# Optimization experiments

Measured on AMD Instinct MI355X. Metric: run time of the kernel, lower is better.

The kernel has to match this reference:

```python
import jax, jax.numpy as jnp
import numpy as np

NUM_LAYERS = 4
INPUT_SIZE = 80
D_MODEL = 512
NHEAD = 8
D_FF = 2048
B = 16
S_MAX = 512
LN_EPS = 1e-5


def setup_inputs() -> dict:
    key = jax.random.key(0)
    ks = jax.random.split(key, 16)
    L, D, F, I = NUM_LAYERS, D_MODEL, D_FF, INPUT_SIZE
    s = 0.02
    inp = {
        "x": jax.random.normal(ks[0], (B, S_MAX, I), dtype=jnp.float32),
        "lens": jax.random.randint(ks[1], (B,), S_MAX // 2, S_MAX + 1, dtype=jnp.int32),
        "We": jax.random.normal(ks[2], (D, I), jnp.float32) * s,
        "be": jnp.zeros((D,), jnp.float32),
        "Wqkv": jax.random.normal(ks[3], (L, 3 * D, D), jnp.float32) * s,
        "bqkv": jnp.zeros((L, 3 * D), jnp.float32),
        "Wo": jax.random.normal(ks[4], (L, D, D), jnp.float32) * s,
        "bo": jnp.zeros((L, D), jnp.float32),
        "ln1_g": jnp.ones((L, D), jnp.float32),
        "ln1_b": jnp.zeros((L, D), jnp.float32),
        "W1": jax.random.normal(ks[5], (L, F, D), jnp.float32) * s,
        "b1": jnp.zeros((L, F), jnp.float32),
        "W2": jax.random.normal(ks[6], (L, D, F), jnp.float32) * s,
        "b2": jnp.zeros((L, D), jnp.float32),
        "ln2_g": jnp.ones((L, D), jnp.float32),
        "ln2_b": jnp.zeros((L, D), jnp.float32),
    }
    return inp


def _layer_norm(x, g, b):
    m = jnp.mean(x, axis=-1, keepdims=True)
    v = jnp.mean(jnp.square(x - m), axis=-1, keepdims=True)
    return (x - m) * jax.lax.rsqrt(v + LN_EPS) * g + b


def _pos_encoding(S, D, dtype):
    pos = jnp.arange(S, dtype=jnp.float32)[:, None]
    div = jnp.exp(jnp.arange(0, D, 2, dtype=jnp.float32) * (-np.log(10000.0) / D))
    pe = jnp.zeros((S, D), jnp.float32)
    pe = pe.at[:, 0::2].set(jnp.sin(pos * div))
    pe = pe.at[:, 1::2].set(jnp.cos(pos * div))
    return pe.astype(dtype)


def _encoder_layer(h, key_mask, Wqkv, bqkv, Wo, bo, g1, b1_, W1, b1f, W2, b2f, g2, b2_):
    # h: [B,S,D], key_mask: [B,S] bool (True = valid). Post-norm (PyTorch default).
    Bq, S, D = h.shape
    dh = D // NHEAD
    qkv = jnp.einsum("bsd,ed->bse", h, Wqkv) + bqkv  # [B,S,3D]
    q, k, v = jnp.split(qkv, 3, axis=-1)
    q = q.reshape(Bq, S, NHEAD, dh).transpose(0, 2, 1, 3)
    k = k.reshape(Bq, S, NHEAD, dh).transpose(0, 2, 1, 3)
    v = v.reshape(Bq, S, NHEAD, dh).transpose(0, 2, 1, 3)
    scores = jnp.einsum("bhqd,bhkd->bhqk", q, k) / jnp.sqrt(jnp.asarray(dh, h.dtype))
    scores = jnp.where(key_mask[:, None, None, :], scores, jnp.asarray(-1e9, h.dtype))
    attn = jax.nn.softmax(scores, axis=-1)
    ctx = jnp.einsum("bhqk,bhkd->bhqd", attn, v)
    ctx = ctx.transpose(0, 2, 1, 3).reshape(Bq, S, D)
    attn_out = jnp.einsum("bsd,ed->bse", ctx, Wo) + bo
    h = _layer_norm(h + attn_out, g1, b1_)
    ff = jnp.einsum("bsf,df->bsd", jax.nn.relu(jnp.einsum("bsd,fd->bsf", h, W1) + b1f), W2) + b2f
    return _layer_norm(h + ff, g2, b2_)


def reference(x, lens, We, be, Wqkv, bqkv, Wo, bo, ln1_g, ln1_b, W1, b1, W2, b2, ln2_g, ln2_b):
    Bq, S, _ = x.shape
    D = We.shape[0]
    h = jnp.einsum("bsi,di->bsd", x, We) + be  # Linear embedding
    h = h + _pos_encoding(S, D, h.dtype)[None]
    key_mask = jnp.arange(S)[None, :] < lens[:, None]  # [B,S]
    for l in range(Wqkv.shape[0]):
        h = _encoder_layer(h, key_mask, Wqkv[l], bqkv[l], Wo[l], bo[l],
                           ln1_g[l], ln1_b[l], W1[l], b1[l], W2[l], b2[l],
                           ln2_g[l], ln2_b[l])
    pooled = jnp.sum(h * key_mask[..., None].astype(h.dtype), axis=1)
    pooled = pooled / lens[:, None].astype(h.dtype)  # mean over valid tokens
    return pooled, lens
```

## Files before the change

kernel.cpp:

```cpp
#include <hip/hip_runtime.h>
#include <math.h>

#define D_MODEL 512
#define NHEAD   8
#define DH      64
#define D_FF    2048
#define BATCH   16
#define SMAX    512
#define NTOK    (BATCH*SMAX)
#define NLAYER  4

constexpr int MODE_RELU = 3;
constexpr int MODE_PART = 4;

typedef __attribute__((ext_vector_type(8))) __bf16 bf16x8;
typedef __attribute__((ext_vector_type(4))) float  f32x4;
typedef __attribute__((ext_vector_type(8))) int    i32x8;
typedef unsigned char u8;

#define WSCALE_INV 0.03125f
#define QSCALE     0.18033688011112042f

__device__ __forceinline__ unsigned short f2bf(float f) {
  union { float f; unsigned u; } v; v.f = f;
  unsigned r = v.u + 0x7FFFu + ((v.u >> 16) & 1u);
  return (unsigned short)(r >> 16);
}
__device__ __forceinline__ float bf2f(unsigned short u) {
  union { unsigned u; float f; } v; v.u = ((unsigned)u) << 16; return v.f;
}
__device__ __forceinline__ int pk4(float a, float b, float c, float d) {
  int t = __builtin_amdgcn_cvt_pk_fp8_f32(a, b, 0, false);
  t = __builtin_amdgcn_cvt_pk_fp8_f32(c, d, t, true);
  return t;
}

__device__ __forceinline__ void gl_lds16(const unsigned short* g, unsigned short* l) {
  __builtin_amdgcn_global_load_lds(
      (const __attribute__((address_space(1))) unsigned int*)g,
      (__attribute__((address_space(3)))       unsigned int*)l, 16, 0, 0);
}
__device__ __forceinline__ void gl_lds16b(const u8* g, u8* l) {
  __builtin_amdgcn_global_load_lds(
      (const __attribute__((address_space(1))) unsigned int*)g,
      (__attribute__((address_space(3)))       unsigned int*)l, 16, 0, 0);
}

__device__ __forceinline__ i32x8 ldfrag(const u8* base, int row, int q) {
  const int rx = row & 7;
  const int4 lo = *(const int4*)(base + (row << 7) + ((((2*q)    ) ^ rx) << 4));
  const int4 hi = *(const int4*)(base + (row << 7) + ((((2*q) + 1) ^ rx) << 4));
  union { int4 p[2]; i32x8 v; } u;
  u.p[0] = lo; u.p[1] = hi;
  return u.v;
}

template<int MODE>
__global__ __launch_bounds__(256)
void gemm_fp8(const u8* __restrict__ A, const u8* __restrict__ Bw,
              const float* __restrict__ bias, u8* __restrict__ C8,
              unsigned short* __restrict__ Cb,
              const int* __restrict__ lens, int K, int CK, int N)
{
  const int lin = blockIdx.x + gridDim.x*(blockIdx.y + gridDim.y*blockIdx.z);
  int m0, n0, kz = 0;
  {
    m0 = (lin % gridDim.y) * 128;
    const int rest = lin / gridDim.y;
    n0 = (rest % gridDim.x) * 128;
    kz = rest / gridDim.x;
  }
  if ((m0 & 511) >= lens[m0 >> 9]) return;

  __shared__ __attribute__((aligned(16))) u8 As[2][16384];
  __shared__ __attribute__((aligned(16))) u8 Bs[2][16384];
  const int tid  = threadIdx.x;
  const int lane = tid & 63;
  const int w    = tid >> 6;
  const int wm   = (w & 1) * 64;
  const int wn   = (w >> 1) * 64;
  const int l15  = lane & 15, quad = lane >> 4;

  f32x4 acc[4][4] = {};

  const int sr  = tid >> 3;
  const int sch = ((tid & 7) ^ (sr & 7)) * 16;
  const u8* Ag = A  + (long)(m0 + sr) * K + kz*CK + sch;
  const u8* Bg = Bw + (long)(n0 + sr) * K + kz*CK + sch;
  const long rowskip = (long)32 * K;
  const int t16 = tid * 16;
  const int niter = CK >> 7;

  auto stage = [&](int t, int bix) {
    const u8* a_ = Ag + t*128;
    const u8* b_ = Bg + t*128;
#pragma unroll
    for (int s = 0; s < 4; s++) {
      gl_lds16b(a_ + s*rowskip, &As[bix][s*4096 + t16]);
      gl_lds16b(b_ + s*rowskip, &Bs[bix][s*4096 + t16]);
    }
  };

  stage(0, 0);
  stage(1, 1);

  for (int it = 0; it < niter; ++it) {
    if (it + 1 < niter)
      asm volatile("s_waitcnt vmcnt(8)\n\ts_barrier" ::: "memory");
    else
      asm volatile("s_waitcnt vmcnt(0)\n\ts_barrier" ::: "memory");

    const int cur = it & 1;
    const u8* Ac = &As[cur][0];
    const u8* Bc = &Bs[cur][0];

    i32x8 bfv[4];
#pragma unroll
    for (int j = 0; j < 4; j++)
      bfv[j] = ldfrag(Bc, wn + j*16 + l15, quad);
#pragma unroll
    for (int i = 0; i < 4; i++) {
      const i32x8 af = ldfrag(Ac, wm + i*16 + l15, quad);
#pragma unroll
      for (int j = 0; j < 4; j++)
        acc[i][j] = __builtin_amdgcn_mfma_scale_f32_16x16x128_f8f6f4(
            af, bfv[j], acc[i][j], 0, 0, 0, 0x7F7F7F7F, 0, 0x7F7F7F7F);
    }

    if (it + 2 < niter) {
      __syncthreads();
      stage(it + 2, cur);
    }
  }

  __syncthreads();
  const int rr8 = lane >> 3, ch8 = lane & 7;

  if (MODE == MODE_RELU) {
    float* epf = (float*)&As[0][0] + w * 1088;
#pragma unroll
    for (int i = 0; i < 4; i++) {
#pragma unroll
      for (int j = 0; j < 4; j++) {
        const float cbv = bias[n0 + wn + j*16 + l15];
#pragma unroll
        for (int r = 0; r < 4; r++)
          epf[(quad*4 + r)*68 + j*16 + l15] = fmaxf(acc[i][j][r]*WSCALE_INV + cbv, 0.f);
      }
      asm volatile("s_waitcnt lgkmcnt(0)" ::: "memory");
      const int row = lane >> 2, c16 = (lane & 3) * 16;
      const float* rp = epf + row*68 + c16;
      f32x4 f0 = *(const f32x4*)(rp + 0);
      f32x4 f1 = *(const f32x4*)(rp + 4);
      f32x4 f2 = *(const f32x4*)(rp + 8);
      f32x4 f3 = *(const f32x4*)(rp + 12);
      int4 o;
      o.x = pk4(f0.x, f0.y, f0.z, f0.w);
      o.y = pk4(f1.x, f1.y, f1.z, f1.w);
      o.z = pk4(f2.x, f2.y, f2.z, f2.w);
      o.w = pk4(f3.x, f3.y, f3.z, f3.w);
      const int mrow = m0 + wm + i*16 + row;
      *(int4*)&C8[(long)mrow*N + n0 + wn + c16] = o;
      asm volatile("s_waitcnt lgkmcnt(0)" ::: "memory");
    }
  } else {
    unsigned short* epi = (unsigned short*)&As[0][0] + w * 1152;
#pragma unroll
    for (int i = 0; i < 4; i++) {
#pragma unroll
      for (int j = 0; j < 4; j++) {
#pragma unroll
        for (int r = 0; r < 4; r++) {
          float v = acc[i][j][r] * WSCALE_INV;
          epi[(quad*4 + r)*72 + j*16 + l15] = f2bf(v);
        }
      }
      asm volatile("s_waitcnt lgkmcnt(0)" ::: "memory");
#pragma unroll
      for (int rs = 0; rs < 2; rs++) {
        const int row  = rs*8 + rr8;
        const int mrow = m0 + wm + i*16 + row;
        bf16x8 val = *(const bf16x8*)&epi[row*72 + ch8*8];
        *(bf16x8*)&Cb[((long)kz*NTOK + mrow)*N + n0 + wn + ch8*8] = val;
      }
      asm volatile("s_waitcnt lgkmcnt(0)" ::: "memory");
    }
  }
}

__global__ __launch_bounds__(256)
void gemm_qkv(const u8* __restrict__ h8, const u8* __restrict__ wq,
              const float* __restrict__ bqkv,
              unsigned short* __restrict__ qd, unsigned short* __restrict__ kd,
              unsigned short* __restrict__ vt_b,
              const int* __restrict__ lens)
{
  const int lin = blockIdx.x;
  const bool isVT = lin >= 512;
  int m0, n0;
  if (isVT) { const int idx = lin - 512; n0 = (idx & 63) * 128; m0 = (idx >> 6) * 128; }
  else      { m0 = (lin & 63) * 128;     n0 = (lin >> 6) * 128; }
  { const int tb = isVT ? n0 : m0;
    if ((tb & 511) >= lens[tb >> 9]) return; }

  const u8* Ap = isVT ? (wq + (long)2*D_MODEL*D_MODEL) : h8;
  const u8* Bp = isVT ? h8 : wq;

  __shared__ __attribute__((aligned(16))) u8 As[2][16384];
  __shared__ __attribute__((aligned(16))) u8 Bs[2][16384];
  const int tid  = threadIdx.x;
  const int lane = tid & 63;
  const int w    = tid >> 6;
  const int wm   = (w & 1) * 64;
  const int wn   = (w >> 1) * 64;
  const int l15  = lane & 15, quad = lane >> 4;

  f32x4 acc[4][4] = {};

  const int sr  = tid >> 3;
  const int sch = ((tid & 7) ^ (sr & 7)) * 16;
  const u8* Ag = Ap + (long)(m0 + sr) * 512 + sch;
  const u8* Bg = Bp + (long)(n0 + sr) * 512 + sch;
  const long rowskip = (long)32 * 512;
  const int t16 = tid * 16;

  auto stage = [&](int t, int bix) {
    const u8* a_ = Ag + t*128;
    const u8* b_ = Bg + t*128;
#pragma unroll
    for (int s = 0; s < 4; s++) {
      gl_lds16b(a_ + s*rowskip, &As[bix][s*4096 + t16]);
      gl_lds16b(b_ + s*rowskip, &Bs[bix][s*4096 + t16]);
    }
  };

  stage(0, 0);
  stage(1, 1);

#pragma unroll 1
  for (int it = 0; it < 4; ++it) {
    if (it + 1 < 4)
      asm volatile("s_waitcnt vmcnt(8)\n\ts_barrier" ::: "memory");
    else
      asm volatile("s_waitcnt vmcnt(0)\n\ts_barrier" ::: "memory");

    const int cur = it & 1;
    const u8* Ac = &As[cur][0];
    const u8* Bc = &Bs[cur][0];

    i32x8 bfv[4];
#pragma unroll
    for (int j = 0; j < 4; j++)
      bfv[j] = ldfrag(Bc, wn + j*16 + l15, quad);
#pragma unroll
    for (int i = 0; i < 4; i++) {
      const i32x8 af = ldfrag(Ac, wm + i*16 + l15, quad);
#pragma unroll
      for (int j = 0; j < 4; j++)
        acc[i][j] = __builtin_amdgcn_mfma_scale_f32_16x16x128_f8f6f4(
            af, bfv[j], acc[i][j], 0, 0, 0, 0x7F7F7F7F, 0, 0x7F7F7F7F);
    }

    if (it + 2 < 4) {
      __syncthreads();
      stage(it + 2, cur);
    }
  }

  __syncthreads();
  const int rr8 = lane >> 3, ch8 = lane & 7;
  unsigned short* epi = (unsigned short*)&As[0][0] + w * 1152;
  const bool isq = !isVT && (((n0 + wn) >> 9) == 0);
#pragma unroll
  for (int i = 0; i < 4; i++) {
    float rbv[4];
    if (isVT) {
#pragma unroll
      for (int r = 0; r < 4; r++) rbv[r] = bqkv[2*D_MODEL + m0 + wm + i*16 + quad*4 + r];
    }
#pragma unroll
    for (int j = 0; j < 4; j++) {
      float cbv = 0.f;
      if (!isVT) cbv = bqkv[n0 + wn + j*16 + l15];
#pragma unroll
      for (int r = 0; r < 4; r++) {
        float v = acc[i][j][r] * WSCALE_INV;
        if (!isVT) { v += cbv; if (isq) v *= QSCALE; }
        else       v += rbv[r];
        epi[(quad*4 + r)*72 + j*16 + l15] = f2bf(v);
      }
    }
    asm volatile("s_waitcnt lgkmcnt(0)" ::: "memory");
#pragma unroll
    for (int rs = 0; rs < 2; rs++) {
      const int row  = rs*8 + rr8;
      const int mrow = m0 + wm + i*16 + row;
      bf16x8 val = *(const bf16x8*)&epi[row*72 + ch8*8];
      if (!isVT) {
        const int nb    = n0 + wn;
        const int which = nb >> 9;
        const int head  = (nb >> 6) & 7;
        unsigned short* dst = which ? kd : qd;
        const int bh = (mrow >> 9)*8 + head;
        *(bf16x8*)&dst[((long)(bh*512 + (mrow & 511)))*64 + ch8*8] = val;
      } else {
        const int head = mrow >> 6, d = mrow & 63;
        const int tok  = n0 + wn + ch8*8;
        const int b    = tok >> 9;
        *(bf16x8*)&vt_b[((long)((b*8 + head)*64 + d))*512 + (tok & 511)] = val;
      }
    }
    asm volatile("s_waitcnt lgkmcnt(0)" ::: "memory");
  }
}

template<int KS>
__global__ __launch_bounds__(256)
void reduce_ln(const unsigned short* __restrict__ part,
               const float* __restrict__ bias,
               const float* __restrict__ g, const float* __restrict__ bb,
               u8* __restrict__ h8, const int* __restrict__ lens)
{
  const int tid  = threadIdx.x;
  const int half = tid >> 7;
  const int t    = tid & 127;
  const int row  = blockIdx.x*2 + half;
  const bool valid = (row & 511) < lens[row >> 9];

  const int hv = ((const int*)(h8 + (long)row*512))[t];
  float4 bs = ((const float4*)bias)[t];
  float v0 = __builtin_amdgcn_cvt_f32_fp8(hv, 0) + bs.x;
  float v1 = __builtin_amdgcn_cvt_f32_fp8(hv, 1) + bs.y;
  float v2 = __builtin_amdgcn_cvt_f32_fp8(hv, 2) + bs.z;
  float v3 = __builtin_amdgcn_cvt_f32_fp8(hv, 3) + bs.w;
#pragma unroll
  for (int z = 0; z < KS; z++) {
    ushort4 p = ((const ushort4*)(part + ((long)z*NTOK + row)*512))[t];
    v0 += bf2f(p.x); v1 += bf2f(p.y); v2 += bf2f(p.z); v3 += bf2f(p.w);
  }
  float s  = v0 + v1 + v2 + v3;
  float s2 = v0*v0 + v1*v1 + v2*v2 + v3*v3;
#pragma unroll
  for (int off = 1; off < 64; off <<= 1) {
    s  += __shfl_xor(s, off);
    s2 += __shfl_xor(s2, off);
  }
  __shared__ float rb[2][2][2];
  if ((t & 63) == 0) { rb[half][t>>6][0] = s; rb[half][t>>6][1] = s2; }
  __syncthreads();
  s  = rb[half][0][0] + rb[half][1][0];
  s2 = rb[half][0][1] + rb[half][1][1];
  const float mean = s * (1.f/512.f);
  const float var  = fmaxf(s2 * (1.f/512.f) - mean*mean, 0.f);
  const float rstd = rsqrtf(var + 1e-5f);
  const float4 gv = ((const float4*)g)[t];
  const float4 bv = ((const float4*)bb)[t];
  const float o0 = (v0-mean)*rstd*gv.x + bv.x;
  const float o1 = (v1-mean)*rstd*gv.y + bv.y;
  const float o2 = (v2-mean)*rstd*gv.z + bv.z;
  const float o3 = (v3-mean)*rstd*gv.w + bv.w;
  if (valid)
    ((int*)(h8 + (long)row*512))[t] = pk4(o0, o1, o2, o3);
}

__global__ __launch_bounds__(256)
void attn_mfma(const unsigned short* __restrict__ qg,
               const unsigned short* __restrict__ kb,
               const unsigned short* __restrict__ vtb,
               const int* __restrict__ lens,
               u8* __restrict__ ctx8)
{
  const int bh = blockIdx.x, qt = blockIdx.y;
  const int b = bh >> 3, hh = bh & 7;
  const int len = lens[b];
  if (qt*64 >= len) return;

  __shared__ __attribute__((aligned(16))) u8 smem[41984];
  unsigned short* Ks0 = (unsigned short*)smem;
  unsigned short* Vts0 = (unsigned short*)(smem + 16384);
  unsigned short* Ps  = (unsigned short*)(smem + 32768);
  const int tid = threadIdx.x;
  const int w = tid >> 6, lane = tid & 63, l15 = lane & 15, quad = lane >> 4;
  const int t8 = tid * 8;

  const int srow = tid >> 2;
  const int s8   = (tid & 3) * 8;
  const unsigned short* Kbase = kb  + ((long)(bh*512 + srow))*64 + s8;
  const unsigned short* Vbase = vtb + ((long)(bh*64 + srow))*512 + s8;

  const unsigned short* qrow = qg + ((long)(bh*512 + qt*64 + w*16 + l15))*64;
  const bf16x8 qf0 = *(const bf16x8*)(qrow + quad*8);
  const bf16x8 qf1 = *(const bf16x8*)(qrow + 32 + quad*8);

  f32x4 O[4] = {};
  float lrow[4] = {0.f,0.f,0.f,0.f};
  unsigned short* Pw = &Ps[w*16*72];
  const int ntiles = (len + 63) >> 6;

  {
    gl_lds16(Kbase,      &Ks0[t8]);
    gl_lds16(Kbase + 32, &Ks0[2048 + t8]);
    gl_lds16(Vbase,      &Vts0[t8]);
    gl_lds16(Vbase + 32, &Vts0[2048 + t8]);
  }

  for (int kt = 0; kt < ntiles; kt++) {
    const int cur = kt & 1;
    unsigned short* Kc  = Ks0  + cur*4096;
    unsigned short* Vc  = Vts0 + cur*4096;
    __syncthreads();
    if (kt + 1 < ntiles) {
      const unsigned short* Kg = Kbase + (long)(kt+1)*64*64;
      const unsigned short* Vg = Vbase + (long)(kt+1)*64;
      unsigned short* Kn = Ks0  + (cur^1)*4096;
      unsigned short* Vn = Vts0 + (cur^1)*4096;
      gl_lds16(Kg,      &Kn[t8]);
      gl_lds16(Kg + 32, &Kn[2048 + t8]);
      gl_lds16(Vg,      &Vn[t8]);
      gl_lds16(Vg + 32, &Vn[2048 + t8]);
    }

    f32x4 sc[4];
#pragma unroll
    for (int ks = 0; ks < 4; ks++) {
      bf16x8 kf0 = *(const bf16x8*)&Kc[       (ks*16 + l15)*32 + quad*8];
      bf16x8 kf1 = *(const bf16x8*)&Kc[2048 + (ks*16 + l15)*32 + quad*8];
      f32x4 z = {};
      z = __builtin_amdgcn_mfma_f32_16x16x32_bf16(qf0, kf0, z, 0, 0, 0);
      sc[ks] = __builtin_amdgcn_mfma_f32_16x16x32_bf16(qf1, kf1, z, 0, 0, 0);
    }

    if (kt*64 + 64 > len) {
#pragma unroll
      for (int ks = 0; ks < 4; ks++) {
        const bool valid = (kt*64 + ks*16 + l15) < len;
#pragma unroll
        for (int r = 0; r < 4; r++)
          sc[ks][r] = valid ? sc[ks][r] : -1e30f;
      }
    }

    float pv[4][4];
#pragma unroll
    for (int ks = 0; ks < 4; ks++)
#pragma unroll
      for (int r = 0; r < 4; r++) {
        const float p = exp2f(sc[ks][r] - 16.f);
        pv[ks][r] = p;
        lrow[r] += p;
      }

#pragma unroll
    for (int ks = 0; ks < 4; ks++)
#pragma unroll
      for (int r = 0; r < 4; r++)
        Pw[(quad*4 + r)*72 + ks*16 + l15] = f2bf(pv[ks][r]);
    asm volatile("s_waitcnt lgkmcnt(0)" ::: "memory");

    const bf16x8 pa0 = *(const bf16x8*)&Pw[l15*72 + quad*8];
    const bf16x8 pa1 = *(const bf16x8*)&Pw[l15*72 + 32 + quad*8];
#pragma unroll
    for (int d = 0; d < 4; d++) {
      bf16x8 vf0 = *(const bf16x8*)&Vc[       (d*16 + l15)*32 + quad*8];
      bf16x8 vf1 = *(const bf16x8*)&Vc[2048 + (d*16 + l15)*32 + quad*8];
      O[d] = __builtin_amdgcn_mfma_f32_16x16x32_bf16(pa0, vf0, O[d], 0, 0, 0);
      O[d] = __builtin_amdgcn_mfma_f32_16x16x32_bf16(pa1, vf1, O[d], 0, 0, 0);
    }
  }

#pragma unroll
  for (int r = 0; r < 4; r++) {
    float t = lrow[r];
    t += __shfl_xor(t, 1);
    t += __shfl_xor(t, 2);
    t += __shfl_xor(t, 4);
    t += __shfl_xor(t, 8);
    lrow[r] = t;
  }

  __syncthreads();
  float* epf = (float*)smem + w * 1088;
#pragma unroll
  for (int r = 0; r < 4; r++) {
    const float inv = 1.f / lrow[r];
#pragma unroll
    for (int d = 0; d < 4; d++)
      epf[(quad*4 + r)*68 + d*16 + l15] = O[d][r] * inv;
  }
  asm volatile("s_waitcnt lgkmcnt(0)" ::: "memory");
  {
    const int row = lane >> 2, c16 = (lane & 3) * 16;
    const float* rp = epf + row*68 + c16;
    f32x4 f0 = *(const f32x4*)(rp + 0);
    f32x4 f1 = *(const f32x4*)(rp + 4);
    f32x4 f2 = *(const f32x4*)(rp + 8);
    f32x4 f3 = *(const f32x4*)(rp + 12);
    int4 o;
    o.x = pk4(f0.x, f0.y, f0.z, f0.w);
    o.y = pk4(f1.x, f1.y, f1.z, f1.w);
    o.z = pk4(f2.x, f2.y, f2.z, f2.w);
    o.w = pk4(f3.x, f3.y, f3.z, f3.w);
    const long gaddr = (long)(b*512 + qt*64 + w*16 + row)*512 + hh*64 + c16;
    *(int4*)&ctx8[gaddr] = o;
  }
}

__global__ __launch_bounds__(256)
void gemm_embed(const float* __restrict__ A, const float* __restrict__ Bm,
                const float* __restrict__ bias,
                u8* __restrict__ C8, int K, int N)
{
  __shared__ float As[8][132];
  __shared__ float Bs[8][68];
  const int tid = threadIdx.x;
  const int m0 = blockIdx.y * 128;
  const int n0 = blockIdx.x * 64;
  const int tx = tid & 15, ty = tid >> 4;
  const int a_k = tid & 7, a_m = tid >> 3;

  float acc[8][4] = {};
  const float* Ag = A  + (long)(m0 + a_m) * K + a_k;
  const float* Bg = Bm + (long)(n0 + a_m) * K + a_k;

  for (int k0 = 0; k0 < K; k0 += 8) {
#pragma unroll
    for (int i = 0; i < 4; i++)
      As[a_k][a_m + 32*i] = Ag[k0 + (long)32*i*K];
#pragma unroll
    for (int i = 0; i < 2; i++)
      Bs[a_k][a_m + 32*i] = Bg[k0 + (long)32*i*K];
    __syncthreads();
#pragma unroll
    for (int kk = 0; kk < 8; kk++) {
      float a[8], bv[4];
#pragma unroll
      for (int r = 0; r < 8; r++) a[r] = As[kk][ty*8 + r];
#pragma unroll
      for (int c = 0; c < 4; c++) bv[c] = Bs[kk][tx*4 + c];
#pragma unroll
      for (int r = 0; r < 8; r++)
#pragma unroll
        for (int c = 0; c < 4; c++)
          acc[r][c] += a[r] * bv[c];
    }
    __syncthreads();
  }

  const int n_base = n0 + tx*4;
  const float cfreq = -13.287712379549449f / 512.0f;
  const float dv0 = exp2f((float)(n_base)     * cfreq);
  const float dv1 = exp2f((float)(n_base + 2) * cfreq);
#pragma unroll
  for (int r = 0; r < 8; r++) {
    int m = m0 + ty*8 + r;
    int s = m & 511;
    float a0 = (float)s * dv0, a1 = (float)s * dv1;
    float s0v, c0v, s1v, c1v;
    __sincosf(a0, &s0v, &c0v);
    __sincosf(a1, &s1v, &c1v);
    int o = pk4(acc[r][0] + bias[n_base+0] + s0v,
                acc[r][1] + bias[n_base+1] + c0v,
                acc[r][2] + bias[n_base+2] + s1v,
                acc[r][3] + bias[n_base+3] + c1v);
    *(int*)(C8 + (long)m*N + n_base) = o;
  }
}

#define N4_QKV (NLAYER*3*D_MODEL*D_MODEL/4)
#define N4_WO  (NLAYER*D_MODEL*D_MODEL/4)
#define N4_W1  (NLAYER*D_FF*D_MODEL/4)
#define N4_W2  (NLAYER*D_MODEL*D_FF/4)
__global__ __launch_bounds__(256)
void cvt_all(const float* __restrict__ wq, const float* __restrict__ wo,
             const float* __restrict__ w1, const float* __restrict__ w2,
             u8* __restrict__ oq, u8* __restrict__ oo,
             u8* __restrict__ o1, u8* __restrict__ o2)
{
  int i = blockIdx.x*256 + threadIdx.x;
  const float* src; u8* dst; int off;
  if (i < N4_QKV)                          { src = wq; dst = oq; off = i; }
  else if (i < N4_QKV + N4_WO)             { src = wo; dst = oo; off = i - N4_QKV; }
  else if (i < N4_QKV + N4_WO + N4_W1)     { src = w1; dst = o1; off = i - N4_QKV - N4_WO; }
  else if (i < N4_QKV + N4_WO + N4_W1 + N4_W2) { src = w2; dst = o2; off = i - N4_QKV - N4_WO - N4_W1; }
  else return;
  float4 v = ((const float4*)src)[off];
  ((int*)dst)[off] = pk4(v.x*32.f, v.y*32.f, v.z*32.f, v.w*32.f);
}

__global__ __launch_bounds__(256)
void out_init(float* __restrict__ out, const int* __restrict__ lens)
{
  int i = blockIdx.x*256 + threadIdx.x;
  if (i < 8192) out[i] = 0.f;
  else if (i < 8192 + 16) out[i] = (float)lens[i - 8192];
}

__global__ __launch_bounds__(256)
void pool_kernel(const u8* __restrict__ h8,
                 const int* __restrict__ lens, float* __restrict__ out)
{
  const int b = blockIdx.y;
  const int s0 = blockIdx.x * 64;
  const int len = lens[b];
  if (s0 >= len) return;
  const int send = min(s0 + 64, len);
  const int tid = threadIdx.x;
  const int c = (tid & 127) * 4;
  const int half = tid >> 7;
  float a0 = 0.f, a1 = 0.f, a2 = 0.f, a3 = 0.f;
  for (int s = s0 + half; s < send; s += 2) {
    const int v = *(const int*)(h8 + ((long)(b*512 + s))*512 + c);
    a0 += __builtin_amdgcn_cvt_f32_fp8(v, 0);
    a1 += __builtin_amdgcn_cvt_f32_fp8(v, 1);
    a2 += __builtin_amdgcn_cvt_f32_fp8(v, 2);
    a3 += __builtin_amdgcn_cvt_f32_fp8(v, 3);
  }
  const float inv = 1.0f / (float)len;
  atomicAdd(out + b*512 + c + 0, a0 * inv);
  atomicAdd(out + b*512 + c + 1, a1 * inv);
  atomicAdd(out + b*512 + c + 2, a2 * inv);
  atomicAdd(out + b*512 + c + 3, a3 * inv);
}

extern "C" void kernel_launch(void* const* d_in, const int* in_sizes, int n_in,
                              void* d_out, int out_size, void* d_ws, size_t ws_size,
                              hipStream_t stream)
{
  const float* x    = (const float*)d_in[0];
  const int*   lens = (const int*)  d_in[1];
  const float* We   = (const float*)d_in[2];
  const float* be   = (const float*)d_in[3];
  const float* Wqkv = (const float*)d_in[4];
  const float* bqkv = (const float*)d_in[5];
  const float* Wo   = (const float*)d_in[6];
  const float* bo   = (const float*)d_in[7];
  const float* ln1g = (const float*)d_in[8];
  const float* ln1b = (const float*)d_in[9];
  const float* W1   = (const float*)d_in[10];
  const float* b1   = (const float*)d_in[11];
  const float* W2   = (const float*)d_in[12];
  const float* b2   = (const float*)d_in[13];
  const float* ln2g = (const float*)d_in[14];
  const float* ln2b = (const float*)d_in[15];
  float* out = (float*)d_out;

  const long TOK_D = (long)NTOK * D_MODEL;
  u8* base = (u8*)d_ws;
  u8* h8    = base + 4*TOK_D;
  u8* ctx8  = h8   + TOK_D;
  u8* ff8   = ctx8 + TOK_D;
  unsigned short* q_b  = (unsigned short*)(ff8 + 4*TOK_D);
  unsigned short* k_b  = q_b + TOK_D;
  unsigned short* vt_b = k_b + TOK_D;
  unsigned short* part = vt_b + TOK_D;
  u8* wq8 = (u8*)(part + 4*TOK_D);
  u8* wo8 = wq8 + (long)NLAYER*3*D_MODEL*D_MODEL;
  u8* w18 = wo8 + (long)NLAYER*D_MODEL*D_MODEL;
  u8* w28 = w18 + (long)NLAYER*D_FF*D_MODEL;

  const dim3 blk(256);

  {
    const int n4tot = N4_QKV + N4_WO + N4_W1 + N4_W2;
    cvt_all<<<dim3((n4tot+255)/256), blk, 0, stream>>>(
        Wqkv, Wo, W1, W2, wq8, wo8, w18, w28);
  }

  gemm_embed<<<dim3(D_MODEL/64, NTOK/128), blk, 0, stream>>>(
      x, We, be, h8, 80, D_MODEL);

  for (int l = 0; l < NLAYER; l++) {
    const u8* wq_l = wq8 + (long)l * 3*D_MODEL * D_MODEL;
    const u8* wo_l = wo8 + (long)l * D_MODEL * D_MODEL;
    const u8* w1_l = w18 + (long)l * D_FF * D_MODEL;
    const u8* w2_l = w28 + (long)l * D_MODEL * D_FF;
    const float* bqkv_l = bqkv + (long)l * 3*D_MODEL;
    const float* bo_l   = bo   + (long)l * D_MODEL;
    const float* b1_l   = b1   + (long)l * D_FF;
    const float* b2_l   = b2   + (long)l * D_MODEL;

    gemm_qkv<<<dim3(768), blk, 0, stream>>>(
        h8, wq_l, bqkv_l, q_b, k_b, vt_b, lens);

    attn_mfma<<<dim3(NHEAD*BATCH, SMAX/64), blk, 0, stream>>>(
        q_b, k_b, vt_b, lens, ctx8);

    gemm_fp8<MODE_PART><<<dim3(D_MODEL/128, NTOK/128, 2), blk, 0, stream>>>(
        ctx8, wo_l, nullptr, nullptr, part, lens,
        D_MODEL, D_MODEL/2, D_MODEL);
    reduce_ln<2><<<dim3(NTOK/2), blk, 0, stream>>>(
        part, bo_l, ln1g + l*D_MODEL, ln1b + l*D_MODEL, h8, lens);

    gemm_fp8<MODE_RELU><<<dim3(D_FF/128, NTOK/128), blk, 0, stream>>>(
        h8, w1_l, b1_l, ff8, nullptr, lens, D_MODEL, D_MODEL, D_FF);

    gemm_fp8<MODE_PART><<<dim3(D_MODEL/128, NTOK/128, 2), blk, 0, stream>>>(
        ff8, w2_l, nullptr, nullptr, part, lens,
        D_FF, D_FF/2, D_MODEL);
    reduce_ln<2><<<dim3(NTOK/2), blk, 0, stream>>>(
        part, b2_l, ln2g + l*D_MODEL, ln2b + l*D_MODEL, h8, lens);
  }

  out_init<<<dim3((8192 + 16 + 255) / 256), blk, 0, stream>>>(out, lens);
  pool_kernel<<<dim3(SMAX/64, BATCH), blk, 0, stream>>>(h8, lens, out);
}
```

Before: 502.5 us.

## Rework attention to 32x32 MFMA tiles with register-resident P and swizzled LDS

The attention kernel now handles 128 query rows per block using 32x32x16 bf16 MFMAs, halving the grid along the query dimension so each K/V tile loaded into LDS is reused by twice as many queries. Softmax probabilities stay in registers and are rearranged with v_permlane32_swap to form the A operand of the PV MFMA, removing the LDS write/read round trip for P. K/V chunks are XOR-swizzled when loaded to cut LDS bank conflicts. In exchange there are fewer blocks, so occupancy on short sequences may drop, and register pressure per thread rises.

```diff
diff --git a/kernel.cpp b/kernel.cpp
--- a/kernel.cpp
+++ b/kernel.cpp
@@ -13,9 +13,10 @@
 constexpr int MODE_RELU = 3;
 constexpr int MODE_PART = 4;
 
-typedef __attribute__((ext_vector_type(8))) __bf16 bf16x8;
-typedef __attribute__((ext_vector_type(4))) float  f32x4;
-typedef __attribute__((ext_vector_type(8))) int    i32x8;
+typedef __attribute__((ext_vector_type(8)))  __bf16 bf16x8;
+typedef __attribute__((ext_vector_type(4)))  float  f32x4;
+typedef __attribute__((ext_vector_type(16))) float  f32x16;
+typedef __attribute__((ext_vector_type(8)))  int    i32x8;
 typedef unsigned char u8;
 
 #define WSCALE_INV 0.03125f
@@ -365,7 +366,7 @@
 
 __global__ __launch_bounds__(256)
 void attn_mfma(const unsigned short* __restrict__ qg,
-               const unsigned short* __restrict__ kb,
+               const unsigned short* __restrict__ kbt,
                const unsigned short* __restrict__ vtb,
                const int* __restrict__ lens,
                u8* __restrict__ ctx8)
@@ -373,41 +374,43 @@
   const int bh = blockIdx.x, qt = blockIdx.y;
   const int b = bh >> 3, hh = bh & 7;
   const int len = lens[b];
-  if (qt*64 >= len) return;
-
-  __shared__ __attribute__((aligned(16))) u8 smem[41984];
-  unsigned short* Ks0 = (unsigned short*)smem;
+  if (qt*128 >= len) return;
+
+  __shared__ __attribute__((aligned(16))) u8 smem[35328];
+  unsigned short* Ks0  = (unsigned short*)smem;
   unsigned short* Vts0 = (unsigned short*)(smem + 16384);
-  unsigned short* Ps  = (unsigned short*)(smem + 32768);
+  float* lden = (float*)(smem + 34816);
+
   const int tid = threadIdx.x;
-  const int w = tid >> 6, lane = tid & 63, l15 = lane & 15, quad = lane >> 4;
+  const int w = tid >> 6, lane = tid & 63;
+  const int l31 = lane & 31, h = lane >> 5;
   const int t8 = tid * 8;
+  const int swz = l31 & 3;
 
   const int srow = tid >> 2;
-  const int s8   = (tid & 3) * 8;
-  const unsigned short* Kbase = kb  + ((long)(bh*512 + srow))*64 + s8;
-  const unsigned short* Vbase = vtb + ((long)(bh*64 + srow))*512 + s8;
-
-  const unsigned short* qrow = qg + ((long)(bh*512 + qt*64 + w*16 + l15))*64;
-  const bf16x8 qf0 = *(const bf16x8*)(qrow + quad*8);
-  const bf16x8 qf1 = *(const bf16x8*)(qrow + 32 + quad*8);
-
-  f32x4 O[4] = {};
-  float lrow[4] = {0.f,0.f,0.f,0.f};
-  unsigned short* Pw = &Ps[w*16*72];
+  const int spos = ((tid & 3) ^ (srow & 3)) * 8;
+  const unsigned short* Kbase = kbt + ((long)(bh*512 + srow))*64  + spos;
+  const unsigned short* Vbase = vtb + ((long)(bh*64  + srow))*512 + spos;
+
+  const unsigned short* qrow = qg + ((long)(bh*512 + qt*128 + w*32 + l31))*64 + h*8;
+  const bf16x8 qf0 = *(const bf16x8*)(qrow);
+  const bf16x8 qf1 = *(const bf16x8*)(qrow + 16);
+  const bf16x8 qf2 = *(const bf16x8*)(qrow + 32);
+  const bf16x8 qf3 = *(const bf16x8*)(qrow + 48);
+
+  f32x16 O0 = {}, O1 = {};
+  float lracc = 0.f;
   const int ntiles = (len + 63) >> 6;
 
-  {
-    gl_lds16(Kbase,      &Ks0[t8]);
-    gl_lds16(Kbase + 32, &Ks0[2048 + t8]);
-    gl_lds16(Vbase,      &Vts0[t8]);
-    gl_lds16(Vbase + 32, &Vts0[2048 + t8]);
-  }
+  gl_lds16(Kbase,      &Ks0[t8]);
+  gl_lds16(Kbase + 32, &Ks0[2048 + t8]);
+  gl_lds16(Vbase,      &Vts0[t8]);
+  gl_lds16(Vbase + 32, &Vts0[2048 + t8]);
 
   for (int kt = 0; kt < ntiles; kt++) {
     const int cur = kt & 1;
-    unsigned short* Kc  = Ks0  + cur*4096;
-    unsigned short* Vc  = Vts0 + cur*4096;
+    unsigned short* Kc = Ks0  + cur*4096;
+    unsigned short* Vc = Vts0 + cur*4096;
     __syncthreads();
     if (kt + 1 < ntiles) {
       const unsigned short* Kg = Kbase + (long)(kt+1)*64*64;
@@ -420,88 +423,100 @@
       gl_lds16(Vg + 32, &Vn[2048 + t8]);
     }
 
-    f32x4 sc[4];
-#pragma unroll
-    for (int ks = 0; ks < 4; ks++) {
-      bf16x8 kf0 = *(const bf16x8*)&Kc[       (ks*16 + l15)*32 + quad*8];
-      bf16x8 kf1 = *(const bf16x8*)&Kc[2048 + (ks*16 + l15)*32 + quad*8];
-      f32x4 z = {};
-      z = __builtin_amdgcn_mfma_f32_16x16x32_bf16(qf0, kf0, z, 0, 0, 0);
-      sc[ks] = __builtin_amdgcn_mfma_f32_16x16x32_bf16(qf1, kf1, z, 0, 0, 0);
-    }
-
-    if (kt*64 + 64 > len) {
-#pragma unroll
-      for (int ks = 0; ks < 4; ks++) {
-        const bool valid = (kt*64 + ks*16 + l15) < len;
-#pragma unroll
-        for (int r = 0; r < 4; r++)
-          sc[ks][r] = valid ? sc[ks][r] : -1e30f;
+    int dw[2][4][2];
+#pragma unroll
+    for (int kb2 = 0; kb2 < 2; kb2++) {
+      f32x16 sc = {};
+      const int krow = (kb2*32 + l31) * 32;
+      const bf16x8 af0 = *(const bf16x8*)&Kc[       krow + ((h      ^ swz) * 8)];
+      sc = __builtin_amdgcn_mfma_f32_32x32x16_bf16(af0, qf0, sc, 0, 0, 0);
+      const bf16x8 af1 = *(const bf16x8*)&Kc[       krow + (((2|h)  ^ swz) * 8)];
+      sc = __builtin_amdgcn_mfma_f32_32x32x16_bf16(af1, qf1, sc, 0, 0, 0);
+      const bf16x8 af2 = *(const bf16x8*)&Kc[2048 + krow + ((h      ^ swz) * 8)];
+      sc = __builtin_amdgcn_mfma_f32_32x32x16_bf16(af2, qf2, sc, 0, 0, 0);
+      const bf16x8 af3 = *(const bf16x8*)&Kc[2048 + krow + (((2|h)  ^ swz) * 8)];
+      sc = __builtin_amdgcn_mfma_f32_32x32x16_bf16(af3, qf3, sc, 0, 0, 0);
+
+      if (kt*64 + kb2*32 + 32 > len) {
+#pragma unroll
+        for (int r = 0; r < 16; r++) {
+          const int kk = kt*64 + kb2*32 + (r & 3) + 8*(r >> 2) + 4*h;
+          sc[r] = (kk < len) ? sc[r] : -1e30f;
+        }
       }
-    }
-
-    float pv[4][4];
-#pragma unroll
-    for (int ks = 0; ks < 4; ks++)
-#pragma unroll
-      for (int r = 0; r < 4; r++) {
-        const float p = exp2f(sc[ks][r] - 16.f);
-        pv[ks][r] = p;
-        lrow[r] += p;
+
+      float p[16];
+#pragma unroll
+      for (int r = 0; r < 16; r++) { p[r] = exp2f(sc[r] - 16.f); lracc += p[r]; }
+#pragma unroll
+      for (int rq = 0; rq < 4; rq++) {
+        dw[kb2][rq][0] = (int)f2bf(p[4*rq+0]) | ((int)f2bf(p[4*rq+1]) << 16);
+        dw[kb2][rq][1] = (int)f2bf(p[4*rq+2]) | ((int)f2bf(p[4*rq+3]) << 16);
       }
-
-#pragma unroll
-    for (int ks = 0; ks < 4; ks++)
-#pragma unroll
-      for (int r = 0; r < 4; r++)
-        Pw[(quad*4 + r)*72 + ks*16 + l15] = f2bf(pv[ks][r]);
-    asm volatile("s_waitcnt lgkmcnt(0)" ::: "memory");
-
-    const bf16x8 pa0 = *(const bf16x8*)&Pw[l15*72 + quad*8];
-    const bf16x8 pa1 = *(const bf16x8*)&Pw[l15*72 + 32 + quad*8];
-#pragma unroll
-    for (int d = 0; d < 4; d++) {
-      bf16x8 vf0 = *(const bf16x8*)&Vc[       (d*16 + l15)*32 + quad*8];
-      bf16x8 vf1 = *(const bf16x8*)&Vc[2048 + (d*16 + l15)*32 + quad*8];
-      O[d] = __builtin_amdgcn_mfma_f32_16x16x32_bf16(pa0, vf0, O[d], 0, 0, 0);
-      O[d] = __builtin_amdgcn_mfma_f32_16x16x32_bf16(pa1, vf1, O[d], 0, 0, 0);
-    }
-  }
-
-#pragma unroll
-  for (int r = 0; r < 4; r++) {
-    float t = lrow[r];
-    t += __shfl_xor(t, 1);
-    t += __shfl_xor(t, 2);
-    t += __shfl_xor(t, 4);
-    t += __shfl_xor(t, 8);
-    lrow[r] = t;
+    }
+
+#pragma unroll
+    for (int kc = 0; kc < 4; kc++) {
+      const int kb2 = kc >> 1;
+      const int rqa = (kc & 1) * 2, rqb = rqa + 1;
+      int a0 = dw[kb2][rqa][0], b0 = dw[kb2][rqb][0];
+      int a1 = dw[kb2][rqa][1], b1 = dw[kb2][rqb][1];
+      asm volatile("v_permlane32_swap_b32 %0, %1" : "+v"(a0), "+v"(b0));
+      asm volatile("v_permlane32_swap_b32 %0, %1" : "+v"(a1), "+v"(b1));
+      union { int d4[4]; bf16x8 v8; } pa;
+      pa.d4[0] = a0; pa.d4[1] = a1; pa.d4[2] = b0; pa.d4[3] = b1;
+      const int chunk = ((((kc & 1) << 1) | h) ^ swz) * 8;
+      const int halfo = (kc >> 1) * 2048;
+      const bf16x8 vf0 = *(const bf16x8*)&Vc[halfo + l31*32 + chunk];
+      const bf16x8 vf1 = *(const bf16x8*)&Vc[halfo + (32 + l31)*32 + chunk];
+      O0 = __builtin_amdgcn_mfma_f32_32x32x16_bf16(pa.v8, vf0, O0, 0, 0, 0);
+      O1 = __builtin_amdgcn_mfma_f32_32x32x16_bf16(pa.v8, vf1, O1, 0, 0, 0);
+    }
+  }
+
+  float lr = lracc + __shfl_xor(lracc, 32);
+  if (h == 0) lden[w*32 + l31] = lr;
+  asm volatile("s_waitcnt lgkmcnt(0)" ::: "memory");
+  f32x4 inv4[4];
+#pragma unroll
+  for (int a = 0; a < 4; a++) {
+    const f32x4 dv = *(const f32x4*)&lden[w*32 + a*8 + h*4];
+    inv4[a] = 1.f / dv;
   }
 
   __syncthreads();
-  float* epf = (float*)smem + w * 1088;
-#pragma unroll
-  for (int r = 0; r < 4; r++) {
-    const float inv = 1.f / lrow[r];
-#pragma unroll
-    for (int d = 0; d < 4; d++)
-      epf[(quad*4 + r)*68 + d*16 + l15] = O[d][r] * inv;
+  float* epf = (float*)smem + w * 2176;
+#pragma unroll
+  for (int r = 0; r < 16; r++) {
+    const int q = (r & 3) + 8*(r >> 2) + 4*h;
+    const float iv = inv4[r >> 2][r & 3];
+    epf[q*68 + l31]      = O0[r] * iv;
+    epf[q*68 + 32 + l31] = O1[r] * iv;
   }
   asm volatile("s_waitcnt lgkmcnt(0)" ::: "memory");
   {
-    const int row = lane >> 2, c16 = (lane & 3) * 16;
-    const float* rp = epf + row*68 + c16;
+    const int row = lane >> 1, ch = (lane & 1) * 32;
+    const float* rp = epf + row*68 + ch;
     f32x4 f0 = *(const f32x4*)(rp + 0);
     f32x4 f1 = *(const f32x4*)(rp + 4);
     f32x4 f2 = *(const f32x4*)(rp + 8);
     f32x4 f3 = *(const f32x4*)(rp + 12);
-    int4 o;
-    o.x = pk4(f0.x, f0.y, f0.z, f0.w);
-    o.y = pk4(f1.x, f1.y, f1.z, f1.w);
-    o.z = pk4(f2.x, f2.y, f2.z, f2.w);
-    o.w = pk4(f3.x, f3.y, f3.z, f3.w);
-    const long gaddr = (long)(b*512 + qt*64 + w*16 + row)*512 + hh*64 + c16;
-    *(int4*)&ctx8[gaddr] = o;
+    f32x4 g0 = *(const f32x4*)(rp + 16);
+    f32x4 g1 = *(const f32x4*)(rp + 20);
+    f32x4 g2 = *(const f32x4*)(rp + 24);
+    f32x4 g3 = *(const f32x4*)(rp + 28);
+    int4 o0, o1;
+    o0.x = pk4(f0.x, f0.y, f0.z, f0.w);
+    o0.y = pk4(f1.x, f1.y, f1.z, f1.w);
+    o0.z = pk4(f2.x, f2.y, f2.z, f2.w);
+    o0.w = pk4(f3.x, f3.y, f3.z, f3.w);
+    o1.x = pk4(g0.x, g0.y, g0.z, g0.w);
+    o1.y = pk4(g1.x, g1.y, g1.z, g1.w);
+    o1.z = pk4(g2.x, g2.y, g2.z, g2.w);
+    o1.w = pk4(g3.x, g3.y, g3.z, g3.w);
+    const long gaddr = (long)(b*512 + qt*128 + w*32 + row)*512 + hh*64 + ch;
+    *(int4*)&ctx8[gaddr]      = o0;
+    *(int4*)&ctx8[gaddr + 16] = o1;
   }
 }
 
@@ -682,7 +697,7 @@
     gemm_qkv<<<dim3(768), blk, 0, stream>>>(
         h8, wq_l, bqkv_l, q_b, k_b, vt_b, lens);
 
-    attn_mfma<<<dim3(NHEAD*BATCH, SMAX/64), blk, 0, stream>>>(
+    attn_mfma<<<dim3(NHEAD*BATCH, SMAX/128), blk, 0, stream>>>(
         q_b, k_b, vt_b, lens, ctx8);
 
     gemm_fp8<MODE_PART><<<dim3(D_MODEL/128, NTOK/128, 2), blk, 0, stream>>>(
```

New measurement: 505.0 us. Within noise of the previous version (+0.5%).
